# Optimization experiments

Hardware: AMD Instinct MI355X
Metric: run time of the kernel (lower is better)

The kernel has to match this reference:

```python
import jax, jax.numpy as jnp
import numpy as np

THR = 0.05          # init kwarg thr
MARGIN = 1.0        # torch TripletMarginLoss default used in module
PD_EPS = 1e-6       # torch pairwise_distance eps (added to the difference)
NORM_EPS = 1e-12    # torch F.normalize eps


def _l2_normalize(X):
    n = jnp.linalg.norm(X, axis=1, keepdims=True)
    return X / jnp.maximum(n, NORM_EPS)


def _pdist(Xn):
    # D[i,j] = || Xn[i] - Xn[j] + eps ||_2, computed without an NxNxd tensor:
    # ||a-b+e||^2 = ||a||^2 + ||b||^2 - 2 a.b + 2e*(sum(a)-sum(b)) + d*e^2
    d = Xn.shape[1]
    s2 = jnp.sum(Xn * Xn, axis=1)
    G = Xn @ Xn.T
    rs = jnp.sum(Xn, axis=1)
    D2 = (s2[:, None] + s2[None, :] - 2.0 * G
          + 2.0 * PD_EPS * (rs[:, None] - rs[None, :]) + d * (PD_EPS ** 2))
    return jnp.sqrt(jnp.maximum(D2, 0.0))


def _forward(Xs):
    # 1) per-view thresholded similarity graphs
    graphs = []
    for X in Xs:
        Xn = _l2_normalize(X)
        S = Xn @ Xn.T
        graphs.append((S > THR).astype(X.dtype))
    # 2) Despite in-place aliasing in the torch code, each view's effective
    #    adjacency is the clipped union of all view graphs minus the diagonal.
    U = jnp.minimum(sum(graphs), 1.0)
    N = U.shape[0]
    A = U - jnp.eye(N, dtype=U.dtype)
    pos_mask = A > 0                      # anchors/positives
    zero_mask = (A == 0)                  # negative candidates (incl. self, as in torch)
    csum = jnp.cumsum(zero_mask.astype(jnp.int32), axis=1)  # [N,N] per-row zero ranks
    cnt = csum[:, -1]                     # negatives per row (>0 w.h.p.)
    key = jax.random.key(42)

    def row_search(c, r):                 # first k with csum[k] > r -> rank-r zero
        return jnp.searchsorted(c, r, side='right')

    total = jnp.asarray(0.0, dtype=Xs[0].dtype)
    for v, X in enumerate(Xs):
        Xn = _l2_normalize(X)
        D = _pdist(Xn)                    # [N,N] anchor-to-all distances
        u = jax.random.uniform(jax.random.fold_in(key, v), (N, N), dtype=jnp.float32)
        r = jnp.minimum((u * cnt[:, None].astype(jnp.float32)).astype(jnp.int32),
                        jnp.maximum(cnt[:, None] - 1, 0))
        n_idx = jax.vmap(row_search)(csum, r)              # [N,N] sampled negative per (i,p)
        d_an = jnp.take_along_axis(D, n_idx, axis=1)
        loss_pair = jnp.maximum(D - d_an + MARGIN, 0.0)    # d(a,p) - d(a,n) + margin
        m = pos_mask.astype(X.dtype)
        total = total + jnp.sum(loss_pair * m) / jnp.sum(m)
    return total


def setup_inputs() -> dict:
    key = jax.random.key(0)
    k0, k1, k2 = jax.random.split(key, 3)
    N, d = 4096, 512
    return {
        "X0": jax.random.normal(k0, (N, d), dtype=jnp.float32),
        "X1": jax.random.normal(k1, (N, d), dtype=jnp.float32),
        "X2": jax.random.normal(k2, (N, d), dtype=jnp.float32),
    }


def reference(X0, X1, X2):
    return _forward([X0, X1, X2])
```

## Files before the change

kernel.cpp:

```cpp
#include <hip/hip_runtime.h>
#include <stdint.h>

#define NROW 4096
#define NDIM 512
#define THRS 0.05f

typedef __attribute__((ext_vector_type(8))) __bf16 bf16x8;
typedef __attribute__((ext_vector_type(4))) float f32x4;

#define XHI_OFF  0ull
#define XHI_SZ   (3ull*4096ull*512ull*2ull)
#define XLO_OFF  (XHI_OFF + XHI_SZ)
#define XLO_SZ   XHI_SZ
#define RT_OFF   (XLO_OFF + XLO_SZ)
#define RT_SZ    (3ull*4096ull*4ull)
#define CT_OFF   (RT_OFF + RT_SZ)
#define CT_SZ    (3ull*4096ull*4ull)
#define G_OFF    (CT_OFF + CT_SZ)
#define G_SZ     (3ull*4096ull*4096ull*4ull)
#define ACC_OFF  (G_OFF + G_SZ)
#define WS_NEEDED (ACC_OFF + 64ull)

__host__ __device__ __forceinline__ void tf2x32(uint32_t k0, uint32_t k1,
                                                uint32_t x0, uint32_t x1,
                                                uint32_t* o0, uint32_t* o1) {
  uint32_t ks2 = k0 ^ k1 ^ 0x1BD11BDAu;
  x0 += k0; x1 += k1;
#define TFR(r) { x0 += x1; x1 = (x1 << (r)) | (x1 >> (32 - (r))); x1 ^= x0; }
  TFR(13) TFR(15) TFR(26) TFR(6)
  x0 += k1; x1 += ks2 + 1u;
  TFR(17) TFR(29) TFR(16) TFR(24)
  x0 += ks2; x1 += k0 + 2u;
  TFR(13) TFR(15) TFR(26) TFR(6)
  x0 += k0; x1 += k1 + 3u;
  TFR(17) TFR(29) TFR(16) TFR(24)
  x0 += k1; x1 += ks2 + 4u;
  TFR(13) TFR(15) TFR(26) TFR(6)
  x0 += ks2; x1 += k0 + 5u;
#undef TFR
  *o0 = x0; *o1 = x1;
}

struct Keys { uint32_t k[6]; };

__global__ __launch_bounds__(128) void norm_kernel(const float* __restrict__ X,
                                                   __bf16* __restrict__ Xhi,
                                                   __bf16* __restrict__ Xlo,
                                                   float* __restrict__ rowT,
                                                   float* __restrict__ colT) {
  const int row = blockIdx.x;
  const int tid = threadIdx.x;
  const int lane = tid & 63, wid = tid >> 6;
  const float4 v = *(const float4*)(X + (size_t)row * NDIM + tid * 4);
  float ss = v.x*v.x + v.y*v.y + v.z*v.z + v.w*v.w;
  #pragma unroll
  for (int off = 32; off; off >>= 1) ss += __shfl_down(ss, off);
  __shared__ float sw[2];
  if (lane == 0) sw[wid] = ss;
  __syncthreads();
  const float tot = sw[0] + sw[1];
  const float den = fmaxf(sqrtf(tot), 1e-12f);
  float n[4];
  n[0] = v.x / den; n[1] = v.y / den; n[2] = v.z / den; n[3] = v.w / den;

  __bf16 hi[4], lo[4];
  #pragma unroll
  for (int e = 0; e < 4; ++e) {
    hi[e] = (__bf16)n[e];
    lo[e] = (__bf16)(n[e] - (float)hi[e]);
  }
  *(ushort4*)(Xhi + (size_t)row * NDIM + tid * 4) = *(ushort4*)hi;
  *(ushort4*)(Xlo + (size_t)row * NDIM + tid * 4) = *(ushort4*)lo;

  float ps = n[0] + n[1] + n[2] + n[3];
  float p2 = n[0]*n[0] + n[1]*n[1] + n[2]*n[2] + n[3]*n[3];
  #pragma unroll
  for (int off = 32; off; off >>= 1) { ps += __shfl_down(ps, off); p2 += __shfl_down(p2, off); }
  __shared__ float sw2[4];
  if (lane == 0) { sw2[wid] = ps; sw2[2 + wid] = p2; }
  __syncthreads();
  if (tid == 0) {
    const float rs = sw2[0] + sw2[1];
    const float s2 = sw2[2] + sw2[3];
    rowT[row] = s2 + 2e-6f * rs + 5.12e-10f;
    colT[row] = s2 - 2e-6f * rs;
  }
}

__global__ __launch_bounds__(256) void gemm_syrk_bf16(const __bf16* __restrict__ XhiBase,
                                                      const __bf16* __restrict__ XloBase,
                                                      float* __restrict__ CBase) {
  const int orig = blockIdx.x;
  const int bx = (orig & 7) * (1584 >> 3) + (orig >> 3);

  const int v = bx / 528;
  const int t = bx - v * 528;
  int bi = (int)((65.0f - sqrtf(4225.0f - 8.0f * (float)t)) * 0.5f);
  while ((bi + 1) * (65 - (bi + 1)) / 2 <= t) ++bi;
  while (bi * (65 - bi) / 2 > t) --bi;
  const int bj = bi + (t - bi * (65 - bi) / 2);

  const __bf16* __restrict__ Ahi = XhiBase + (size_t)v * NROW * NDIM;
  const __bf16* __restrict__ Alo = XloBase + (size_t)v * NROW * NDIM;
  float* __restrict__ C = CBase + ((size_t)v << 24);

  __shared__ __align__(16) char smemRaw[34816];
  __bf16 (*As)[64] = (__bf16 (*)[64])smemRaw;
  __bf16 (*Bs)[64] = (__bf16 (*)[64])(smemRaw + 16384);

  const int tid = threadIdx.x;
  const int lane = tid & 63;
  const int wid = tid >> 6;
  const int wr = wid >> 1, wc = wid & 1;

  f32x4 zero4 = {0.f, 0.f, 0.f, 0.f};
  f32x4 acc[4][4];
  #pragma unroll
  for (int m = 0; m < 4; ++m)
    #pragma unroll
    for (int n = 0; n < 4; ++n) acc[m][n] = zero4;

  const int lrow = lane >> 3;
  const int lcol = (lane & 7) * 8;
  const int fr = lane & 15;
  const int fk = (lane >> 4) * 8;

  for (int kt = 0; kt < 1536; kt += 64) {
    const int s = kt >> 9;
    const int colk = kt & 511;
    const __bf16* __restrict__ Asrc = (s < 2) ? Ahi : Alo;
    const __bf16* __restrict__ Bsrc = (s == 1) ? Alo : Ahi;
    #pragma unroll
    for (int p = 0; p < 4; ++p) {
      const int c = wid * 4 + p;
      const int trow = c * 8 + lrow;
      const __bf16* ga = Asrc + (((size_t)(bi * 128 + trow)) << 9) + colk + lcol;
      const __bf16* gb = Bsrc + (((size_t)(bj * 128 + trow)) << 9) + colk + lcol;
      __builtin_amdgcn_global_load_lds((const __attribute__((address_space(1))) void*)ga,
                                       (__attribute__((address_space(3))) void*)(smemRaw + c * 1024),
                                       16, 0, 0);
      __builtin_amdgcn_global_load_lds((const __attribute__((address_space(1))) void*)gb,
                                       (__attribute__((address_space(3))) void*)(smemRaw + 16384 + c * 1024),
                                       16, 0, 0);
    }
    __syncthreads();
    #pragma unroll
    for (int kk = 0; kk < 64; kk += 32) {
      bf16x8 af[4], bfr[4];
      #pragma unroll
      for (int m = 0; m < 4; ++m)
        af[m] = *(const bf16x8*)&As[wr * 64 + m * 16 + fr][kk + fk];
      #pragma unroll
      for (int n = 0; n < 4; ++n)
        bfr[n] = *(const bf16x8*)&Bs[wc * 64 + n * 16 + fr][kk + fk];
      #pragma unroll
      for (int m = 0; m < 4; ++m)
        #pragma unroll
        for (int n = 0; n < 4; ++n)
          acc[m][n] = __builtin_amdgcn_mfma_f32_16x16x32_bf16(af[m], bfr[n], acc[m][n], 0, 0, 0);
    }
    __syncthreads();
  }

  const int cl = lane & 15;
  const int rg = (lane >> 4) * 4;
  float (*Ls)[136] = (float (*)[136])smemRaw;
  float (*Lt)[68]  = (float (*)[68])smemRaw;

  __syncthreads();
  #pragma unroll
  for (int r = 0; r < 2; ++r) {
    if (r) __syncthreads();
    if (wr == r) {
      #pragma unroll
      for (int m = 0; m < 4; ++m)
        #pragma unroll
        for (int n = 0; n < 4; ++n)
          #pragma unroll
          for (int q = 0; q < 4; ++q)
            Ls[m * 16 + rg + q][wc * 64 + n * 16 + cl] = acc[m][n][q];
    }
    __syncthreads();
    #pragma unroll
    for (int q = 0; q < 8; ++q) {
      const int idx = q * 256 + tid;
      const int row = idx >> 5, c4 = idx & 31;
      *(float4*)&C[(size_t)(bi * 128 + r * 64 + row) * NROW + bj * 128 + c4 * 4] =
          *(const float4*)&Ls[row][c4 * 4];
    }
    if (bi != bj) {
      __syncthreads();
      if (wr == r) {
        #pragma unroll
        for (int m = 0; m < 4; ++m)
          #pragma unroll
          for (int n = 0; n < 4; ++n)
            #pragma unroll
            for (int q = 0; q < 4; ++q)
              Lt[wc * 64 + n * 16 + cl][m * 16 + rg + q] = acc[m][n][q];
      }
      __syncthreads();
      #pragma unroll
      for (int q = 0; q < 8; ++q) {
        const int idx = q * 256 + tid;
        const int mrow = idx >> 4, c4 = idx & 15;
        *(float4*)&C[(size_t)(bj * 128 + mrow) * NROW + bi * 128 + r * 64 + c4 * 4] =
            *(const float4*)&Lt[mrow][c4 * 4];
      }
    }
  }
}

__global__ __launch_bounds__(256, 4) void loss_kernel(const float* __restrict__ G,
                                                      const float* __restrict__ rowT,
                                                      const float* __restrict__ colT,
                                                      double* __restrict__ lossAcc,
                                                      unsigned long long* __restrict__ posAcc,
                                                      Keys keys) {
  __shared__ float sBuf[NROW];
  __shared__ unsigned short zlist[NROW];
  __shared__ unsigned short plist[NROW];
  __shared__ unsigned char nib[1024];
  __shared__ int sWaveTot[4];
  __shared__ float sLoss[4];

  const int i = blockIdx.x;
  const int tid = threadIdx.x;
  const int lane = tid & 63, wid = tid >> 6;

  {
    bool posb[4][4];
    #pragma unroll
    for (int p = 0; p < 4; ++p) {
      const int j4 = p * 1024 + tid * 4;
      #pragma unroll
      for (int e = 0; e < 4; ++e) posb[p][e] = false;
      #pragma unroll
      for (int v = 0; v < 3; ++v) {
        const float4 g = *(const float4*)(G + ((size_t)v << 24) + ((size_t)i << 12) + j4);
        posb[p][0] |= (g.x > THRS); posb[p][1] |= (g.y > THRS);
        posb[p][2] |= (g.z > THRS); posb[p][3] |= (g.w > THRS);
      }
      unsigned int z = 0;
      #pragma unroll
      for (int e = 0; e < 4; ++e) {
        const int j = j4 + e;
        const bool pos = posb[p][e] && (j != i);
        if (!pos) z |= (1u << e);
      }
      nib[p * 256 + tid] = (unsigned char)z;
    }
  }
  __syncthreads();

  const uchar4 myn = *(const uchar4*)&nib[tid * 4];
  const int cz = __popc((unsigned)myn.x) + __popc((unsigned)myn.y) +
                 __popc((unsigned)myn.z) + __popc((unsigned)myn.w);
  int inc = cz;
  #pragma unroll
  for (int off = 1; off < 64; off <<= 1) {
    const int s = __shfl_up(inc, off);
    if (lane >= off) inc += s;
  }
  if (lane == 63) sWaveTot[wid] = inc;
  __syncthreads();
  int base = inc - cz;
  for (int w = 0; w < wid; ++w) base += sWaveTot[w];
  const int cnt = sWaveTot[0] + sWaveTot[1] + sWaveTot[2] + sWaveTot[3];
  {
    int zr = base;
    const unsigned char nn[4] = { myn.x, myn.y, myn.z, myn.w };
    #pragma unroll
    for (int q = 0; q < 4; ++q) {
      const int jb = tid * 16 + q * 4;
      #pragma unroll
      for (int e = 0; e < 4; ++e) {
        const int j = jb + e;
        if ((nn[q] >> e) & 1) { zlist[zr] = (unsigned short)j; ++zr; }
        else                  { plist[j - zr] = (unsigned short)j; }
      }
    }
  }
  __syncthreads();

  const int npos = NROW - cnt;
  const float cntf = (float)cnt;
  const int cm1 = cnt - 1;
  float lossSum = 0.0f;

  #pragma unroll
  for (int v = 0; v < 3; ++v) {
    const float rT = rowT[v * NROW + i];
    const float* __restrict__ cT = colT + v * NROW;
    const float* __restrict__ g = G + ((size_t)v << 24) + ((size_t)i << 12);
    #pragma unroll
    for (int p = 0; p < 4; ++p) {
      const int j4 = p * 1024 + tid * 4;
      const float4 gg = *(const float4*)(g + j4);
      const float4 ct = *(const float4*)(cT + j4);
      float4 d;
      d.x = sqrtf(fmaxf((rT + ct.x) - 2.0f * gg.x, 0.0f));
      d.y = sqrtf(fmaxf((rT + ct.y) - 2.0f * gg.y, 0.0f));
      d.z = sqrtf(fmaxf((rT + ct.z) - 2.0f * gg.z, 0.0f));
      d.w = sqrtf(fmaxf((rT + ct.w) - 2.0f * gg.w, 0.0f));
      *(float4*)&sBuf[j4] = d;
    }
    __syncthreads();

    const uint32_t fk0 = keys.k[2 * v], fk1 = keys.k[2 * v + 1];
    const uint32_t tbase = (uint32_t)i * 4096u;
    for (int k = tid; k < npos; k += 256) {
      const int j = plist[k];
      const uint32_t t32 = tbase + (uint32_t)j;
      uint32_t y0, y1, bits;
      if (i < 2048) { tf2x32(fk0, fk1, t32, t32 + 8388608u, &y0, &y1); bits = y0; }
      else          { tf2x32(fk0, fk1, t32 - 8388608u, t32, &y0, &y1); bits = y1; }
      const float u = __uint_as_float((bits >> 9) | 0x3F800000u) - 1.0f;
      int r = (int)(u * cntf);
      r = min(r, cm1);
      const int n = zlist[r];
      lossSum += fmaxf(sBuf[j] - sBuf[n] + 1.0f, 0.0f);
    }
    __syncthreads();
  }

  #pragma unroll
  for (int off = 32; off; off >>= 1) lossSum += __shfl_down(lossSum, off);
  if (lane == 0) sLoss[wid] = lossSum;
  __syncthreads();
  if (tid == 0) {
    const double tot = (double)sLoss[0] + (double)sLoss[1] + (double)sLoss[2] + (double)sLoss[3];
    atomicAdd(lossAcc, tot);
    atomicAdd(posAcc, (unsigned long long)npos);
  }
}

__global__ void finalize_kernel(const double* __restrict__ lossAcc,
                                const unsigned long long* __restrict__ posAcc,
                                float* __restrict__ out) {
  if (threadIdx.x == 0 && blockIdx.x == 0) {
    out[0] = (float)(lossAcc[0] / (double)posAcc[0]);
  }
}

extern "C" void kernel_launch(void* const* d_in, const int* in_sizes, int n_in,
                              void* d_out, int out_size, void* d_ws, size_t ws_size,
                              hipStream_t stream) {
  if (ws_size < WS_NEEDED) return;

  const float* Xs[3] = { (const float*)d_in[0], (const float*)d_in[1], (const float*)d_in[2] };
  char* ws = (char*)d_ws;
  __bf16* Xhi = (__bf16*)(ws + XHI_OFF);
  __bf16* Xlo = (__bf16*)(ws + XLO_OFF);
  float* rowT = (float*)(ws + RT_OFF);
  float* colT = (float*)(ws + CT_OFF);
  float* G  = (float*)(ws + G_OFF);
  double* lossAcc = (double*)(ws + ACC_OFF);
  unsigned long long* posAcc = (unsigned long long*)(ws + ACC_OFF + 8);
  float* out = (float*)d_out;

  hipMemsetAsync(ws + ACC_OFF, 0, 16, stream);

  for (int v = 0; v < 3; ++v)
    norm_kernel<<<NROW, 128, 0, stream>>>(Xs[v],
                                          Xhi + (size_t)v * NROW * NDIM,
                                          Xlo + (size_t)v * NROW * NDIM,
                                          rowT + v * NROW, colT + v * NROW);

  gemm_syrk_bf16<<<3 * 528, 256, 0, stream>>>(Xhi, Xlo, G);

  Keys keys;
  for (uint32_t v = 0; v < 3; ++v) {
    uint32_t y0, y1;
    tf2x32(0u, 42u, 0u, v, &y0, &y1);
    keys.k[2 * v] = y0; keys.k[2 * v + 1] = y1;
  }

  loss_kernel<<<NROW, 256, 0, stream>>>(G, rowT, colT, lossAcc, posAcc, keys);
  finalize_kernel<<<1, 1, 0, stream>>>(lossAcc, posAcc, out);
}
```

Measured before the change: 359.1 us.

## Double-buffer SYRK K-loop with async global-to-LDS prefetch

Replaces the single-buffered 64-wide K tile loop in the bf16 SYRK GEMM with a two-stage, 32-wide K pipeline. The next stage's global_load_lds is issued before computing the current buffer, and a partial vmcnt wait lets memory traffic overlap the MFMA work. The cost is twice as many barriers per K element and less MFMA work per stage. There is also a possible LDS bank-conflict change from the 32-element row stride.

```diff
diff --git a/kernel.cpp b/kernel.cpp
--- a/kernel.cpp
+++ b/kernel.cpp
@@ -94,19 +94,17 @@
   const int bx = (orig & 7) * (1584 >> 3) + (orig >> 3);
 
   const int v = bx / 528;
-  const int t = bx - v * 528;
-  int bi = (int)((65.0f - sqrtf(4225.0f - 8.0f * (float)t)) * 0.5f);
-  while ((bi + 1) * (65 - (bi + 1)) / 2 <= t) ++bi;
-  while (bi * (65 - bi) / 2 > t) --bi;
-  const int bj = bi + (t - bi * (65 - bi) / 2);
+  const int t4 = bx - v * 528;
+  int bi = (int)((65.0f - sqrtf(4225.0f - 8.0f * (float)t4)) * 0.5f);
+  while ((bi + 1) * (65 - (bi + 1)) / 2 <= t4) ++bi;
+  while (bi * (65 - bi) / 2 > t4) --bi;
+  const int bj = bi + (t4 - bi * (65 - bi) / 2);
 
   const __bf16* __restrict__ Ahi = XhiBase + (size_t)v * NROW * NDIM;
   const __bf16* __restrict__ Alo = XloBase + (size_t)v * NROW * NDIM;
   float* __restrict__ C = CBase + ((size_t)v << 24);
 
   __shared__ __align__(16) char smemRaw[34816];
-  __bf16 (*As)[64] = (__bf16 (*)[64])smemRaw;
-  __bf16 (*Bs)[64] = (__bf16 (*)[64])(smemRaw + 16384);
 
   const int tid = threadIdx.x;
   const int lane = tid & 63;
@@ -120,47 +118,66 @@
     #pragma unroll
     for (int n = 0; n < 4; ++n) acc[m][n] = zero4;
 
-  const int lrow = lane >> 3;
-  const int lcol = (lane & 7) * 8;
+  const int srow = wid * 32 + (lane >> 2);
+  const int scol = (lane & 3) * 8;
   const int fr = lane & 15;
   const int fk = (lane >> 4) * 8;
 
-  for (int kt = 0; kt < 1536; kt += 64) {
-    const int s = kt >> 9;
-    const int colk = kt & 511;
-    const __bf16* __restrict__ Asrc = (s < 2) ? Ahi : Alo;
-    const __bf16* __restrict__ Bsrc = (s == 1) ? Alo : Ahi;
-    #pragma unroll
-    for (int p = 0; p < 4; ++p) {
-      const int c = wid * 4 + p;
-      const int trow = c * 8 + lrow;
-      const __bf16* ga = Asrc + (((size_t)(bi * 128 + trow)) << 9) + colk + lcol;
-      const __bf16* gb = Bsrc + (((size_t)(bj * 128 + trow)) << 9) + colk + lcol;
-      __builtin_amdgcn_global_load_lds((const __attribute__((address_space(1))) void*)ga,
-                                       (__attribute__((address_space(3))) void*)(smemRaw + c * 1024),
-                                       16, 0, 0);
-      __builtin_amdgcn_global_load_lds((const __attribute__((address_space(1))) void*)gb,
-                                       (__attribute__((address_space(3))) void*)(smemRaw + 16384 + c * 1024),
-                                       16, 0, 0);
-    }
-    __syncthreads();
-    #pragma unroll
-    for (int kk = 0; kk < 64; kk += 32) {
-      bf16x8 af[4], bfr[4];
-      #pragma unroll
-      for (int m = 0; m < 4; ++m)
-        af[m] = *(const bf16x8*)&As[wr * 64 + m * 16 + fr][kk + fk];
-      #pragma unroll
-      for (int n = 0; n < 4; ++n)
-        bfr[n] = *(const bf16x8*)&Bs[wc * 64 + n * 16 + fr][kk + fk];
-      #pragma unroll
-      for (int m = 0; m < 4; ++m)
-        #pragma unroll
-        for (int n = 0; n < 4; ++n)
-          acc[m][n] = __builtin_amdgcn_mfma_f32_16x16x32_bf16(af[m], bfr[n], acc[m][n], 0, 0, 0);
-    }
-    __syncthreads();
-  }
+  #define STAGE(st, b)                                                                   \
+    {                                                                                    \
+      const int s_ = (st) >> 4;                                                          \
+      const int ck_ = ((st) & 15) * 32;                                                  \
+      const __bf16* As_ = (s_ < 2) ? Ahi : Alo;                                          \
+      const __bf16* Bs_ = (s_ == 1) ? Alo : Ahi;                                         \
+      _Pragma("unroll")                                                                  \
+      for (int h = 0; h < 2; ++h) {                                                      \
+        const __bf16* ga = As_ + (((size_t)(bi * 128 + srow + h * 16)) << 9) + ck_ + scol; \
+        const __bf16* gb = Bs_ + (((size_t)(bj * 128 + srow + h * 16)) << 9) + ck_ + scol; \
+        __builtin_amdgcn_global_load_lds(                                                \
+            (const __attribute__((address_space(1))) void*)ga,                           \
+            (__attribute__((address_space(3))) void*)(smemRaw + (b) * 16384 +            \
+                                                      (wid * 32 + h * 16) * 64),         \
+            16, 0, 0);                                                                   \
+        __builtin_amdgcn_global_load_lds(                                                \
+            (const __attribute__((address_space(1))) void*)gb,                           \
+            (__attribute__((address_space(3))) void*)(smemRaw + (b) * 16384 + 8192 +     \
+                                                      (wid * 32 + h * 16) * 64),         \
+            16, 0, 0);                                                                   \
+      }                                                                                  \
+    }
+
+  #define COMPUTE(b)                                                                     \
+    {                                                                                    \
+      const __bf16(*Ab)[32] = (const __bf16(*)[32])(smemRaw + (b) * 16384);              \
+      const __bf16(*Bb)[32] = (const __bf16(*)[32])(smemRaw + (b) * 16384 + 8192);       \
+      bf16x8 af[4], bfr[4];                                                              \
+      _Pragma("unroll")                                                                  \
+      for (int m = 0; m < 4; ++m) af[m] = *(const bf16x8*)&Ab[wr * 64 + m * 16 + fr][fk];\
+      _Pragma("unroll")                                                                  \
+      for (int n = 0; n < 4; ++n) bfr[n] = *(const bf16x8*)&Bb[wc * 64 + n * 16 + fr][fk];\
+      _Pragma("unroll")                                                                  \
+      for (int m = 0; m < 4; ++m)                                                        \
+        _Pragma("unroll")                                                                \
+        for (int n = 0; n < 4; ++n)                                                      \
+          acc[m][n] = __builtin_amdgcn_mfma_f32_16x16x32_bf16(af[m], bfr[n], acc[m][n],  \
+                                                              0, 0, 0);                  \
+    }
+
+  STAGE(0, 0)
+
+  for (int st = 0; st < 47; ++st) {
+    STAGE(st + 1, (st + 1) & 1)
+    asm volatile("s_waitcnt vmcnt(4)" ::: "memory");
+    __syncthreads();
+    COMPUTE(st & 1)
+    __syncthreads();
+  }
+  asm volatile("s_waitcnt vmcnt(0)" ::: "memory");
+  __syncthreads();
+  COMPUTE(1)
+
+  #undef STAGE
+  #undef COMPUTE
 
   const int cl = lane & 15;
   const int rg = (lane >> 4) * 4;
```

Result: slower. 369.7 us (+2.9%).
